# Kernel optimization log

Hardware: AMD Instinct MI355X
Metric: run time of the kernel (lower is better)

## Reference

```python
import jax, jax.numpy as jnp
import numpy as np

DIM = 1024
HEADS = 16
HEAD_DIM = DIM // HEADS
HIDDEN = 4096  # mlp_ratio * dim
SCALE = HEAD_DIM ** -0.5
LN_EPS = 1e-5


def softmax_one(x):
    # softmax with +1 in the denominator (after max subtraction), per source
    m = jnp.max(x, axis=-1, keepdims=True)
    e = jnp.exp(x - m)
    return e / (1.0 + jnp.sum(e, axis=-1, keepdims=True))


def layer_norm(x, g, b):
    mu = jnp.mean(x, axis=-1, keepdims=True)
    var = jnp.mean(jnp.square(x - mu), axis=-1, keepdims=True)
    return (x - mu) * jax.lax.rsqrt(var + LN_EPS) * g + b


def setup_inputs() -> dict:
    key = jax.random.key(0)
    ks = jax.random.split(key, 12)
    B, C, N = 2, DIM, 2048
    x = jax.random.normal(ks[0], (B, C, N), dtype=jnp.float32)
    mask = jax.random.randint(ks[1], (B, HEADS, N), 0, 2, dtype=jnp.int32)
    s = 0.02
    return {
        'x': x,
        'mask': mask,
        'qkv_w': jax.random.normal(ks[2], (3 * DIM, DIM), jnp.float32) * s,
        'qkv_b': jnp.zeros((3 * DIM,), jnp.float32),
        'proj_w': jax.random.normal(ks[3], (DIM, DIM), jnp.float32) * s,
        'proj_b': jnp.zeros((DIM,), jnp.float32),
        'fc1_w': jax.random.normal(ks[4], (HIDDEN, DIM), jnp.float32) * s,
        'fc1_b': jnp.zeros((HIDDEN,), jnp.float32),
        'ln_g': jnp.ones((HIDDEN,), jnp.float32),
        'ln_b': jnp.zeros((HIDDEN,), jnp.float32),
        'fc2_w': jax.random.normal(ks[5], (DIM, HIDDEN), jnp.float32) * s,
        'fc2_b': jnp.zeros((DIM,), jnp.float32),
    }


def reference(x, mask, qkv_w, qkv_b, proj_w, proj_b, fc1_w, fc1_b, ln_g, ln_b, fc2_w, fc2_b):
    B, C, N = x.shape
    xt = jnp.swapaxes(x, 1, 2)  # (B, N, C)

    # ----- attention -----
    qkv = xt @ qkv_w.T + qkv_b                      # (B, N, 3C)
    qkv = qkv.reshape(B, N, 3, HEADS, HEAD_DIM)
    qkv = jnp.transpose(qkv, (2, 0, 3, 1, 4))       # (3, B, H, N, Dh)
    q, k, v = qkv[0], qkv[1], qkv[2]
    scores = jnp.einsum('bhnd,bhmd->bhnm', q * SCALE, k)  # (B, H, N, N)
    scores = jnp.where(mask[:, :, :, None] == 0, -1e9, scores)
    attn = softmax_one(scores)
    out = jnp.einsum('bhnm,bhmd->bhnd', attn, v)    # (B, H, N, Dh)
    # faithful to source: permute(0,3,1,2).reshape(B,N,C) -> scrambled merge
    out = jnp.transpose(out, (0, 3, 1, 2)).reshape(B, N, C)
    out = out @ proj_w.T + proj_b

    # faithful residual: attn_out + ls1(attn_out) with ls1 = Identity
    h = out + out                                   # (B, N, C)

    # ----- MLP (timm Mlp: fc1 -> GELU -> LayerNorm -> fc2) -----
    m = h @ fc1_w.T + fc1_b
    m = jax.nn.gelu(m, approximate=False)
    m = layer_norm(m, ln_g, ln_b)
    m = m @ fc2_w.T + fc2_b
    y = h + m                                       # (B, N, C)

    return jnp.swapaxes(y, 1, 2)                    # (B, C, N)
```

## Files before the change

### kernel.cpp

```cpp
#include <hip/hip_runtime.h>
#include <math.h>

#define DIMC   1024
#define NTOK   2048
#define BATCH  2
#define HEADS  16
#define HDIM   64
#define HIDDEN 4096
#define MROWS  (BATCH*NTOK)
#define QSZ    ((size_t)BATCH*HEADS*NTOK*HDIM)
#define QSC    0.18033688f

typedef unsigned short ushort_t;
typedef __attribute__((ext_vector_type(8))) short short8;
typedef __attribute__((ext_vector_type(4))) float f32x4;
typedef __attribute__((ext_vector_type(4))) unsigned short us4;

__device__ __forceinline__ ushort_t f2b(float f) {
  union { float f; unsigned int u; } cv; cv.f = f;
  unsigned int u = cv.u;
  unsigned int r = (u + 0x7fffu + ((u >> 16) & 1u)) >> 16;
  return (ushort_t)r;
}

__device__ __forceinline__ float b2f(ushort_t b) {
  union { unsigned int u; float f; } cv; cv.u = ((unsigned int)b) << 16;
  return cv.f;
}

__device__ __forceinline__ float fexp2(float x) {
#if __has_builtin(__builtin_amdgcn_exp2f)
  return __builtin_amdgcn_exp2f(x);
#else
  return exp2f(x);
#endif
}

__device__ __forceinline__ void gl_lds16(const void* g, void* l) {
  __builtin_amdgcn_global_load_lds(
      (const __attribute__((address_space(1))) void*)g,
      (__attribute__((address_space(3))) void*)l, 16, 0, 0);
}

__global__ __launch_bounds__(256) void k_pre(const float* __restrict__ x,
                                             const float* __restrict__ w0,
                                             const float* __restrict__ w1,
                                             const float* __restrict__ w2,
                                             const float* __restrict__ w3,
                                             ushort_t* __restrict__ xt,
                                             ushort_t* __restrict__ o0,
                                             ushort_t* __restrict__ o1,
                                             ushort_t* __restrict__ o2,
                                             ushort_t* __restrict__ o3) {
  __shared__ float t[32][33];
  int bid = blockIdx.x;
  if (bid < 4096) {
    int b   = bid >> 11;
    int rem = bid & 2047;
    int n0  = (rem & 63) * 32;
    int c0  = (rem >> 6) * 32;
    int tx = threadIdx.x & 31, ty = threadIdx.x >> 5;
#pragma unroll
    for (int l = 0; l < 4; l++)
      t[ty + l * 8][tx] = x[((size_t)(b * DIMC + c0 + ty + l * 8)) * NTOK + n0 + tx];
    __syncthreads();
#pragma unroll
    for (int l = 0; l < 4; l++)
      xt[((size_t)(b * NTOK + n0 + ty + l * 8)) * DIMC + c0 + tx] = f2b(t[tx][ty + l * 8]);
  } else {
    int cb = bid - 4096;
    const float* in; ushort_t* out; int base;
    if (cb < 3072)      { in = w0; out = o0; base = cb; }
    else if (cb < 4096) { in = w1; out = o1; base = cb - 3072; }
    else if (cb < 8192) { in = w2; out = o2; base = cb - 4096; }
    else                { in = w3; out = o3; base = cb - 8192; }
    int i = base * 256 + threadIdx.x;
    float4 v = ((const float4*)in)[i];
    us4 o; o.x = f2b(v.x); o.y = f2b(v.y); o.z = f2b(v.z); o.w = f2b(v.w);
    ((us4*)out)[i] = o;
  }
}

template <int EPI, int NTX8, int KSTRIDE, int KLEN, int XROW>
__global__ __launch_bounds__(256) void k_gemm_bf16(const ushort_t* __restrict__ A,
                                                   const ushort_t* __restrict__ W,
                                                   const float* __restrict__ bias,
                                                   void* __restrict__ outv) {
  __shared__ ushort_t As[2][128 * 32];
  __shared__ ushort_t Bs[2][128 * 32];
  const int tid = threadIdx.x;
  const int lane = tid & 63, wv = tid >> 6;
  const int bid = blockIdx.x, kz = blockIdx.y;
  const int xcd = bid & 7, t = bid >> 3;
  const int row0 = XROW ? (xcd * NTX8 + (t % NTX8)) * 128 : (t / NTX8) * 128;
  const int col0 = XROW ? (t / NTX8) * 128 : (xcd * NTX8 + (t % NTX8)) * 128;
  const int wrow0 = (wv >> 1) * 64, wcol0 = (wv & 1) * 64;
  const int lm = lane & 15, lq = lane >> 4;
  const int srow = wv * 32 + (lane >> 2);
  const int gch = (lane & 3) ^ ((lane >> 3) & 3);
  const int sw8 = (lq ^ ((lm >> 1) & 3)) * 8;

  const ushort_t* Ab = A + (size_t)(row0 + srow) * KSTRIDE + (size_t)kz * KLEN + gch * 8;
  const ushort_t* Wb = W + (size_t)(col0 + srow) * KSTRIDE + (size_t)kz * KLEN + gch * 8;
  const size_t rstep = (size_t)16 * KSTRIDE;

  f32x4 acc[4][4];
#pragma unroll
  for (int i = 0; i < 4; i++)
#pragma unroll
    for (int j = 0; j < 4; j++) acc[i][j] = (f32x4){0.f, 0.f, 0.f, 0.f};

#define STAGE(buf, k0) do {                                      \
    gl_lds16(Ab + (k0),         &As[buf][wv * 1024]);            \
    gl_lds16(Ab + rstep + (k0), &As[buf][wv * 1024 + 512]);      \
    gl_lds16(Wb + (k0),         &Bs[buf][wv * 1024]);            \
    gl_lds16(Wb + rstep + (k0), &Bs[buf][wv * 1024 + 512]);      \
  } while (0)

  auto compute = [&](int buf) {
    short8 af[4], bf[4];
#pragma unroll
    for (int mi = 0; mi < 4; mi++)
      af[mi] = *(const short8*)&As[buf][(wrow0 + mi * 16 + lm) * 32 + sw8];
#pragma unroll
    for (int ni = 0; ni < 4; ni++)
      bf[ni] = *(const short8*)&Bs[buf][(wcol0 + ni * 16 + lm) * 32 + sw8];
#pragma unroll
    for (int mi = 0; mi < 4; mi++)
#pragma unroll
      for (int ni = 0; ni < 4; ni++)
        acc[mi][ni] = __builtin_amdgcn_mfma_f32_16x16x32_bf16(af[mi], bf[ni], acc[mi][ni], 0, 0, 0);
  };

  constexpr int S = KLEN / 32;
  STAGE(0, 0);
#pragma unroll 1
  for (int kk = 0; kk < S; kk++) {
    __syncthreads();
    if (kk + 1 < S) STAGE((kk + 1) & 1, (kk + 1) * 32);
    compute(kk & 1);
  }
#undef STAGE

#pragma unroll
  for (int mi = 0; mi < 4; mi++) {
#pragma unroll
    for (int ni = 0; ni < 4; ni++) {
#pragma unroll
      for (int r = 0; r < 4; r++) {
        const int row = row0 + wrow0 + mi * 16 + lq * 4 + r;
        const int col = col0 + wcol0 + ni * 16 + lm;
        float v = acc[mi][ni][r];
        if (EPI != 4) v += bias[col];
        if (EPI == 0) {
          int which = col >> 10, rem = col & 1023, hh = rem >> 6, d = rem & 63;
          int bb = row >> 11, n = row & 2047;
          size_t bh = (size_t)(bb * HEADS + hh);
          ushort_t* o16 = (ushort_t*)outv;
          if (which == 0)
            o16[(bh * NTOK + n) * HDIM + d] = f2b(v * QSC);
          else if (which == 1)
            o16[QSZ + (bh * NTOK + n) * HDIM + d] = f2b(v);
          else
            o16[2 * QSZ + (bh * HDIM + d) * NTOK + n] = f2b(v);
        } else if (EPI == 2) {
          ((ushort_t*)outv)[(size_t)row * HIDDEN + col] = f2b(v);
        } else {
          ((ushort_t*)outv)[(size_t)kz * MROWS * DIMC + (size_t)row * DIMC + col] = f2b(v);
        }
      }
    }
  }
}

__global__ __launch_bounds__(256) void k_comb_proj(const ushort_t* __restrict__ p0,
                                                   const ushort_t* __restrict__ p1,
                                                   const float* __restrict__ bias,
                                                   ushort_t* __restrict__ hb) {
  int i = blockIdx.x * 256 + threadIdx.x;
  int colb = (i & 255) * 4;
  us4 a = ((const us4*)p0)[i];
  us4 b = ((const us4*)p1)[i];
  us4 o;
  o.x = f2b(2.f * (b2f(a.x) + b2f(b.x) + bias[colb + 0]));
  o.y = f2b(2.f * (b2f(a.y) + b2f(b.y) + bias[colb + 1]));
  o.z = f2b(2.f * (b2f(a.z) + b2f(b.z) + bias[colb + 2]));
  o.w = f2b(2.f * (b2f(a.w) + b2f(b.w) + bias[colb + 3]));
  ((us4*)hb)[i] = o;
}

__global__ __launch_bounds__(256) void k_comb_fc2(const ushort_t* __restrict__ p0,
                                                  const ushort_t* __restrict__ p1,
                                                  const ushort_t* __restrict__ hb,
                                                  const float* __restrict__ bias,
                                                  float* __restrict__ out) {
  __shared__ float t[32][33];
  int b  = blockIdx.z;
  int c0 = blockIdx.y * 32, n0 = blockIdx.x * 32;
  int tx = threadIdx.x, ty = threadIdx.y;
#pragma unroll
  for (int l = 0; l < 4; l++) {
    size_t idx = ((size_t)(b * NTOK + n0 + ty + l * 8)) * DIMC + c0 + tx;
    t[ty + l * 8][tx] = b2f(p0[idx]) + b2f(p1[idx]) + b2f(hb[idx]) + bias[c0 + tx];
  }
  __syncthreads();
#pragma unroll
  for (int l = 0; l < 4; l++)
    out[((size_t)(b * DIMC + c0 + ty + l * 8)) * NTOK + n0 + tx] = t[tx][ty + l * 8];
}

__global__ __launch_bounds__(256) void k_attn_mfma(const ushort_t* __restrict__ qkv,
                                                   const int* __restrict__ mask,
                                                   ushort_t* __restrict__ scram) {
  __shared__ ushort_t Kl[2][64 * 64];
  __shared__ ushort_t Vl[2][64 * 64];
  __shared__ ushort_t Pl[4 * 32 * 72];
  const int tid = threadIdx.x;
  const int lane = tid & 63, w = tid >> 6;
  const int lm = lane & 15, quad = lane >> 4;
  const int bh = blockIdx.y, b = bh >> 4, h = bh & 15;
  const int q0 = blockIdx.x * 128 + w * 32;
  const ushort_t* qg  = qkv + (size_t)bh * NTOK * HDIM;
  const ushort_t* kg  = qkv + QSZ + (size_t)bh * NTOK * HDIM;
  const ushort_t* vTg = qkv + 2 * QSZ + (size_t)bh * HDIM * NTOK;
  ushort_t* Pw = &Pl[w * 32 * 72];

  const short8 ones = {0x3F80, 0x3F80, 0x3F80, 0x3F80, 0x3F80, 0x3F80, 0x3F80, 0x3F80};

  short8 qf[2][2];
#pragma unroll
  for (int qs = 0; qs < 2; qs++)
#pragma unroll
    for (int hf = 0; hf < 2; hf++)
      qf[qs][hf] = *(const short8*)&qg[(size_t)(q0 + qs * 16 + lm) * HDIM + hf * 32 + quad * 8];

  bool mk[2][4];
#pragma unroll
  for (int qs = 0; qs < 2; qs++)
#pragma unroll
    for (int r = 0; r < 4; r++)
      mk[qs][r] = mask[(size_t)bh * NTOK + q0 + qs * 16 + quad * 4 + r] != 0;

  f32x4 O[2][4], La[2];
#pragma unroll
  for (int qs = 0; qs < 2; qs++) {
    La[qs] = (f32x4){0.f, 0.f, 0.f, 0.f};
#pragma unroll
    for (int r = 0; r < 4; r++) O[qs][r] = (f32x4){0.f, 0.f, 0.f, 0.f};
  }

  const int s0 = tid, s1 = tid + 256;
  const int r0 = s0 >> 3, g0 = (s0 & 7) ^ (r0 & 7);
  const int r1 = s1 >> 3, g1 = (s1 & 7) ^ (r1 & 7);

  gl_lds16(kg + (size_t)r0 * HDIM + g0 * 8, &Kl[0][s0 * 8]);
  gl_lds16(kg + (size_t)r1 * HDIM + g1 * 8, &Kl[0][s1 * 8]);
  gl_lds16(vTg + (size_t)r0 * NTOK + g0 * 8, &Vl[0][s0 * 8]);
  gl_lds16(vTg + (size_t)r1 * NTOK + g1 * 8, &Vl[0][s1 * 8]);

  for (int kt = 0; kt < NTOK; kt += 64) {
    const int cur = (kt >> 6) & 1, nxt = cur ^ 1;
    __syncthreads();
    if (kt + 64 < NTOK) {
      gl_lds16(kg + (size_t)(kt + 64 + r0) * HDIM + g0 * 8, &Kl[nxt][s0 * 8]);
      gl_lds16(kg + (size_t)(kt + 64 + r1) * HDIM + g1 * 8, &Kl[nxt][s1 * 8]);
      gl_lds16(vTg + (size_t)r0 * NTOK + kt + 64 + g0 * 8, &Vl[nxt][s0 * 8]);
      gl_lds16(vTg + (size_t)r1 * NTOK + kt + 64 + g1 * 8, &Vl[nxt][s1 * 8]);
    }

    short8 kf[4][2];
#pragma unroll
    for (int ksub = 0; ksub < 4; ksub++)
#pragma unroll
      for (int hf = 0; hf < 2; hf++)
        kf[ksub][hf] = *(const short8*)&Kl[cur][(ksub * 16 + lm) * 64 + ((4 * hf + quad) ^ (lm & 7)) * 8];

#pragma unroll
    for (int qs = 0; qs < 2; qs++) {
      f32x4 S[4];
#pragma unroll
      for (int ksub = 0; ksub < 4; ksub++) {
        S[ksub] = (f32x4){0.f, 0.f, 0.f, 0.f};
        S[ksub] = __builtin_amdgcn_mfma_f32_16x16x32_bf16(qf[qs][0], kf[ksub][0], S[ksub], 0, 0, 0);
        S[ksub] = __builtin_amdgcn_mfma_f32_16x16x32_bf16(qf[qs][1], kf[ksub][1], S[ksub], 0, 0, 0);
      }
#pragma unroll
      for (int r = 0; r < 4; r++) {
        const int prow = qs * 16 + quad * 4 + r;
#pragma unroll
        for (int ksub = 0; ksub < 4; ksub++) {
          float p = mk[qs][r] ? fexp2(S[ksub][r]) : 1.0f;
          Pw[prow * 72 + ksub * 16 + lm] = (ushort_t)(__float_as_uint(p) >> 16);
        }
      }
    }
    __builtin_amdgcn_s_waitcnt(0xC07F);

    short8 vf[4][2];
#pragma unroll
    for (int dsub = 0; dsub < 4; dsub++)
#pragma unroll
      for (int hf = 0; hf < 2; hf++)
        vf[dsub][hf] = *(const short8*)&Vl[cur][(dsub * 16 + lm) * 64 + ((4 * hf + quad) ^ (lm & 7)) * 8];

#pragma unroll
    for (int qs = 0; qs < 2; qs++) {
      short8 pf[2];
#pragma unroll
      for (int hf = 0; hf < 2; hf++)
        pf[hf] = *(const short8*)&Pw[(qs * 16 + lm) * 72 + hf * 32 + quad * 8];
#pragma unroll
      for (int dsub = 0; dsub < 4; dsub++) {
        O[qs][dsub] = __builtin_amdgcn_mfma_f32_16x16x32_bf16(pf[0], vf[dsub][0], O[qs][dsub], 0, 0, 0);
        O[qs][dsub] = __builtin_amdgcn_mfma_f32_16x16x32_bf16(pf[1], vf[dsub][1], O[qs][dsub], 0, 0, 0);
      }
      La[qs] = __builtin_amdgcn_mfma_f32_16x16x32_bf16(pf[0], ones, La[qs], 0, 0, 0);
      La[qs] = __builtin_amdgcn_mfma_f32_16x16x32_bf16(pf[1], ones, La[qs], 0, 0, 0);
    }
  }

#pragma unroll
  for (int qs = 0; qs < 2; qs++)
#pragma unroll
    for (int r = 0; r < 4; r++) {
      int n = q0 + qs * 16 + quad * 4 + r;
      float inv = 1.f / (1.f + La[qs][r]);
      int n1 = n >> 10, nn0 = n & 1023;
#pragma unroll
      for (int dsub = 0; dsub < 4; dsub++) {
        int d = dsub * 16 + lm;
        int np = d * 32 + h * 2 + n1;
        scram[((size_t)(b * NTOK + np)) * DIMC + nn0] = f2b(O[qs][dsub][r] * inv);
      }
    }
}

__global__ __launch_bounds__(256) void k_ln(ushort_t* __restrict__ mid,
                                            const float* __restrict__ g,
                                            const float* __restrict__ bta) {
  const int row = blockIdx.x;
  ushort_t* p = mid + (size_t)row * HIDDEN;
  const int tid = threadIdx.x;
  float lv[16];
  float s = 0.f, s2 = 0.f;
#pragma unroll
  for (int i = 0; i < 4; i++) {
    us4 u = *(const us4*)&p[tid * 4 + i * 1024];
#pragma unroll
    for (int j = 0; j < 4; j++) {
      float xx = b2f((j == 0) ? u.x : (j == 1) ? u.y : (j == 2) ? u.z : u.w);
      xx = 0.5f * xx * (1.f + erff(xx * 0.70710678118654752f));
      lv[i * 4 + j] = xx;
      s += xx;
      s2 += xx * xx;
    }
  }
#pragma unroll
  for (int off = 32; off > 0; off >>= 1) {
    s += __shfl_down(s, off);
    s2 += __shfl_down(s2, off);
  }
  __shared__ float rs[4], rs2[4];
  if ((tid & 63) == 0) { rs[tid >> 6] = s; rs2[tid >> 6] = s2; }
  __syncthreads();
  float ts = rs[0] + rs[1] + rs[2] + rs[3];
  float ts2 = rs2[0] + rs2[1] + rs2[2] + rs2[3];
  float mu = ts * (1.f / HIDDEN);
  float var = ts2 * (1.f / HIDDEN) - mu * mu;
  float rstd = rsqrtf(var + 1e-5f);
#pragma unroll
  for (int i = 0; i < 4; i++) {
    us4 o;
#pragma unroll
    for (int j = 0; j < 4; j++) {
      int f = tid * 4 + i * 1024 + j;
      float y = (lv[i * 4 + j] - mu) * rstd * g[f] + bta[f];
      ushort_t ob = f2b(y);
      if (j == 0) o.x = ob; else if (j == 1) o.y = ob; else if (j == 2) o.z = ob; else o.w = ob;
    }
    *(us4*)&p[tid * 4 + i * 1024] = o;
  }
}

extern "C" void kernel_launch(void* const* d_in, const int* in_sizes, int n_in,
                              void* d_out, int out_size, void* d_ws, size_t ws_size,
                              hipStream_t stream) {
  const float* x      = (const float*)d_in[0];
  const int*   mask   = (const int*)d_in[1];
  const float* qkv_w  = (const float*)d_in[2];
  const float* qkv_b  = (const float*)d_in[3];
  const float* proj_w = (const float*)d_in[4];
  const float* proj_b = (const float*)d_in[5];
  const float* fc1_w  = (const float*)d_in[6];
  const float* fc1_b  = (const float*)d_in[7];
  const float* ln_g   = (const float*)d_in[8];
  const float* ln_b   = (const float*)d_in[9];
  const float* fc2_w  = (const float*)d_in[10];
  const float* fc2_b  = (const float*)d_in[11];

  char* w = (char*)d_ws;
  ushort_t* qkv16  = (ushort_t*)w;           w += 3 * QSZ * 2;
  ushort_t* xtb    = (ushort_t*)w;           w += (size_t)MROWS * DIMC * 2;
  ushort_t* scramb = (ushort_t*)w;           w += (size_t)MROWS * DIMC * 2;
  ushort_t* hb     = (ushort_t*)w;           w += (size_t)MROWS * DIMC * 2;
  ushort_t* mid    = (ushort_t*)w;           w += (size_t)MROWS * HIDDEN * 2;
  ushort_t* wqkvb  = (ushort_t*)w;           w += (size_t)3 * DIMC * DIMC * 2;
  ushort_t* wprojb = (ushort_t*)w;           w += (size_t)DIMC * DIMC * 2;
  ushort_t* wfc1b  = (ushort_t*)w;           w += (size_t)HIDDEN * DIMC * 2;
  ushort_t* wfc2b  = (ushort_t*)w;           w += (size_t)DIMC * HIDDEN * 2;
  ushort_t* pbuf   = (ushort_t*)w;           w += (size_t)2 * MROWS * DIMC * 2;
  ushort_t* pbuf1  = pbuf + (size_t)MROWS * DIMC;

  k_pre<<<dim3(4096 + 12288), 256, 0, stream>>>(x, qkv_w, proj_w, fc1_w, fc2_w,
                                                xtb, wqkvb, wprojb, wfc1b, wfc2b);

  k_gemm_bf16<0, 4, DIMC, DIMC, 1><<<dim3(24 * 32), 256, 0, stream>>>(
      xtb, wqkvb, qkv_b, qkv16);
  k_attn_mfma<<<dim3(NTOK / 128, BATCH * HEADS), 256, 0, stream>>>(
      qkv16, mask, scramb);
  k_gemm_bf16<4, 4, DIMC, 512, 1><<<dim3(8 * 32, 2), 256, 0, stream>>>(
      scramb, wprojb, nullptr, pbuf);
  k_comb_proj<<<dim3(4096), 256, 0, stream>>>(pbuf, pbuf1, proj_b, hb);
  k_gemm_bf16<2, 4, DIMC, DIMC, 0><<<dim3(32 * 32), 256, 0, stream>>>(
      hb, wfc1b, fc1_b, mid);
  k_ln<<<dim3(MROWS), 256, 0, stream>>>(mid, ln_g, ln_b);
  k_gemm_bf16<4, 4, HIDDEN, 2048, 1><<<dim3(8 * 32, 2), 256, 0, stream>>>(
      mid, wfc2b, nullptr, pbuf);
  k_comb_fc2<<<dim3(NTOK / 32, DIMC / 32, BATCH), dim3(32, 8), 0, stream>>>(
      pbuf, pbuf1, hb, fc2_b, (float*)d_out);
}
```

Baseline: 360.4 us.

## Add dedicated 256x256-tile fc1 GEMM kernel with staged LDS pipeline

Replaces the generic bf16 GEMM for fc1 with a specialized kernel using 256x256 output tiles, 512 threads (8 waves), double-buffered LDS fed by direct global-to-LDS loads, an XOR-swizzled layout and interleaved sub-tile MFMA phases with s_setprio. The larger tile raises arithmetic intensity and cuts global traffic. Loads for the next k-step are issued between MFMA quarters to overlap memory with compute. The cost is 128KB of LDS per block, heavy register use for 32 accumulators, and only 256 blocks, which may limit occupancy and wave balance across the 256 CUs.

```diff
diff --git a/kernel.cpp b/kernel.cpp
--- a/kernel.cpp
+++ b/kernel.cpp
@@ -163,14 +163,136 @@
             o16[QSZ + (bh * NTOK + n) * HDIM + d] = f2b(v);
           else
             o16[2 * QSZ + (bh * HDIM + d) * NTOK + n] = f2b(v);
-        } else if (EPI == 2) {
-          ((ushort_t*)outv)[(size_t)row * HIDDEN + col] = f2b(v);
         } else {
           ((ushort_t*)outv)[(size_t)kz * MROWS * DIMC + (size_t)row * DIMC + col] = f2b(v);
         }
       }
     }
   }
+}
+
+__global__ __launch_bounds__(512, 2) void k_gemm256_fc1(const ushort_t* __restrict__ A,
+                                                        const ushort_t* __restrict__ W,
+                                                        const float* __restrict__ bias,
+                                                        ushort_t* __restrict__ out) {
+  __shared__ ushort_t As[2][256 * 64];
+  __shared__ ushort_t Bs[2][256 * 64];
+  const int tid = threadIdx.x;
+  const int lane = tid & 63, wid = tid >> 6;
+  const int wr = wid >> 2, wc = wid & 3;
+  const int lm = lane & 15, quad = lane >> 4;
+  const int bid = blockIdx.x;
+  const int lin = (bid & 7) * 32 + (bid >> 3);
+  const int row0 = (lin >> 4) * 256, col0 = (lin & 15) * 256;
+  const int swz = lm & 7;
+
+  const int gch = (tid & 7) ^ ((tid >> 3) & 7);
+  const ushort_t* Ab = A + (size_t)(row0 + (tid >> 3)) * 1024 + gch * 8;
+  const ushort_t* Wb = W + (size_t)(col0 + (tid >> 3)) * 1024 + gch * 8;
+  const int dbase = wid * 512;
+
+  auto stA = [&](int buf, int half, int kt) {
+    const ushort_t* s = Ab + (size_t)(half * 128) * 1024 + kt * 64;
+    gl_lds16(s,             &As[buf][half * 8192 + dbase]);
+    gl_lds16(s + 64 * 1024, &As[buf][half * 8192 + 4096 + dbase]);
+  };
+  auto stB = [&](int buf, int half, int kt) {
+    const ushort_t* s = Wb + (size_t)(half * 128) * 1024 + kt * 64;
+    gl_lds16(s,             &Bs[buf][half * 8192 + dbase]);
+    gl_lds16(s + 64 * 1024, &Bs[buf][half * 8192 + 4096 + dbase]);
+  };
+
+  f32x4 acc[8][4];
+#pragma unroll
+  for (int i = 0; i < 8; i++)
+#pragma unroll
+    for (int j = 0; j < 4; j++) acc[i][j] = (f32x4){0.f, 0.f, 0.f, 0.f};
+
+  short8 af[4][2], bf[4][2];
+
+  auto rdAf = [&](int buf, int mih) {
+#pragma unroll
+    for (int mi = 0; mi < 4; mi++)
+#pragma unroll
+      for (int ks = 0; ks < 2; ks++)
+        af[mi][ks] = *(const short8*)&As[buf][(wr * 128 + (mih * 4 + mi) * 16 + lm) * 64 +
+                                             (((ks * 4 + quad) ^ swz) * 8)];
+  };
+  auto rdBf = [&](int buf, int nh) {
+#pragma unroll
+    for (int nn = 0; nn < 2; nn++)
+#pragma unroll
+      for (int ks = 0; ks < 2; ks++)
+        bf[nh * 2 + nn][ks] = *(const short8*)&Bs[buf][(wc * 64 + (nh * 2 + nn) * 16 + lm) * 64 +
+                                                       (((ks * 4 + quad) ^ swz) * 8)];
+  };
+  auto quadMM = [&](int m0, int n0) {
+    __builtin_amdgcn_s_setprio(1);
+#pragma unroll
+    for (int mi = 0; mi < 4; mi++)
+#pragma unroll
+      for (int ni = 0; ni < 2; ni++)
+#pragma unroll
+        for (int ks = 0; ks < 2; ks++)
+          acc[m0 + mi][n0 + ni] = __builtin_amdgcn_mfma_f32_16x16x32_bf16(
+              af[mi][ks], bf[n0 + ni][ks], acc[m0 + mi][n0 + ni], 0, 0, 0);
+    __builtin_amdgcn_s_setprio(0);
+  };
+
+  constexpr int NT = 16;
+  stB(0, 0, 0); stB(0, 1, 0);
+  stA(0, 0, 0); stA(0, 1, 0);
+  stB(1, 0, 1); stB(1, 1, 1);
+
+#pragma unroll 1
+  for (int kt = 0; kt < NT; kt++) {
+    const int buf = kt & 1;
+    if (kt + 1 < NT) __builtin_amdgcn_s_waitcnt(0x0F74);
+    else             __builtin_amdgcn_s_waitcnt(0x0F70);
+    __builtin_amdgcn_s_barrier();
+    asm volatile("" ::: "memory");
+
+    rdAf(buf, 0);
+    rdBf(buf, 0);
+    if (kt + 1 < NT) stA(buf ^ 1, 0, kt + 1);
+    asm volatile("" ::: "memory");
+    __builtin_amdgcn_s_barrier();
+    quadMM(0, 0);
+    __builtin_amdgcn_s_barrier();
+    asm volatile("" ::: "memory");
+
+    rdBf(buf, 1);
+    if (kt + 1 < NT) stA(buf ^ 1, 1, kt + 1);
+    asm volatile("" ::: "memory");
+    __builtin_amdgcn_s_barrier();
+    quadMM(0, 2);
+    __builtin_amdgcn_s_barrier();
+    asm volatile("" ::: "memory");
+
+    rdAf(buf, 1);
+    if (kt + 2 < NT) stB(buf, 0, kt + 2);
+    asm volatile("" ::: "memory");
+    __builtin_amdgcn_s_barrier();
+    quadMM(4, 2);
+    __builtin_amdgcn_s_barrier();
+    asm volatile("" ::: "memory");
+
+    if (kt + 2 < NT) stB(buf, 1, kt + 2);
+    asm volatile("" ::: "memory");
+    __builtin_amdgcn_s_barrier();
+    quadMM(4, 0);
+  }
+
+#pragma unroll
+  for (int mi = 0; mi < 8; mi++)
+#pragma unroll
+    for (int ni = 0; ni < 4; ni++)
+#pragma unroll
+      for (int r = 0; r < 4; r++) {
+        const int row = row0 + wr * 128 + mi * 16 + quad * 4 + r;
+        const int col = col0 + wc * 64 + ni * 16 + lm;
+        out[(size_t)row * HIDDEN + col] = f2b(acc[mi][ni][r] + bias[col]);
+      }
 }
 
 __global__ __launch_bounds__(256) void k_comb_proj(const ushort_t* __restrict__ p0,
@@ -421,8 +543,7 @@
   k_gemm_bf16<4, 4, DIMC, 512, 1><<<dim3(8 * 32, 2), 256, 0, stream>>>(
       scramb, wprojb, nullptr, pbuf);
   k_comb_proj<<<dim3(4096), 256, 0, stream>>>(pbuf, pbuf1, proj_b, hb);
-  k_gemm_bf16<2, 4, DIMC, DIMC, 0><<<dim3(32 * 32), 256, 0, stream>>>(
-      hb, wfc1b, fc1_b, mid);
+  k_gemm256_fc1<<<dim3(256), 512, 0, stream>>>(hb, wfc1b, fc1_b, mid);
   k_ln<<<dim3(MROWS), 256, 0, stream>>>(mid, ln_g, ln_b);
   k_gemm_bf16<4, 4, HIDDEN, 2048, 1><<<dim3(8 * 32, 2), 256, 0, stream>>>(
       mid, wfc2b, nullptr, pbuf);
```

Result: faster. 344.4 us (-4.4%).
